# Optimization experiments

Measured on AMD Instinct MI355X. Metric: run time of the kernel, lower is better.

## Reference

```python
import jax, jax.numpy as jnp
import numpy as np

NUM_HEADS = 12


def setup_inputs() -> dict:
    key = jax.random.key(0)
    ks = jax.random.split(key, 6)
    B, T, D = 512, 128, 768  # batch, seq (<= CONTEXT_LENGTH=128), d_model
    d_in, d_out = D, D
    s_in = 1.0 / np.sqrt(d_in)
    s_out = 1.0 / np.sqrt(d_out)
    return {
        "x": jax.random.normal(ks[0], (B, T, d_in), dtype=jnp.float32),
        "Wq": jax.random.uniform(ks[1], (d_in, d_out), jnp.float32, -s_in, s_in),
        "Wk": jax.random.uniform(ks[2], (d_in, d_out), jnp.float32, -s_in, s_in),
        "Wv": jax.random.uniform(ks[3], (d_in, d_out), jnp.float32, -s_in, s_in),
        "Wo": jax.random.uniform(ks[4], (d_out, d_out), jnp.float32, -s_out, s_out),
        "bo": jax.random.uniform(ks[5], (d_out,), jnp.float32, -s_out, s_out),
    }


def reference(x, Wq, Wk, Wv, Wo, bo):
    B, T, _ = x.shape
    H = NUM_HEADS
    hd = Wq.shape[1] // H
    # projections -> [b, h, t, hd]
    q = jnp.einsum("btd,de->bte", x, Wq).reshape(B, T, H, hd).transpose(0, 2, 1, 3)
    k = jnp.einsum("btd,de->bte", x, Wk).reshape(B, T, H, hd).transpose(0, 2, 1, 3)
    v = jnp.einsum("btd,de->bte", x, Wv).reshape(B, T, H, hd).transpose(0, 2, 1, 3)
    scores = jnp.einsum("bhqd,bhkd->bhqk", q, k)
    causal = jnp.tril(jnp.ones((T, T), dtype=bool))  # True = keep
    scores = jnp.where(causal, scores, -jnp.inf)
    attn = jax.nn.softmax(scores / jnp.sqrt(jnp.float32(hd)), axis=-1)
    # dropout is identity in eval mode
    ctx = jnp.einsum("bhqk,bhkd->bhqd", attn, v)
    ctx = ctx.transpose(0, 2, 1, 3).reshape(B, T, H * hd)
    return jnp.einsum("btd,de->bte", ctx, Wo) + bo
```

## Files before the change

### kernel.cpp

```cpp
#include <hip/hip_runtime.h>
#include <hip/hip_bf16.h>
#include <cstdint>
#include <math.h>


typedef __bf16 bf16;
typedef __bf16 bf16x8 __attribute__((ext_vector_type(8)));
typedef float f32x4 __attribute__((ext_vector_type(4)));

#define MFMA16(a, b, c) __builtin_amdgcn_mfma_f32_16x16x32_bf16((a), (b), (c), 0, 0, 0)

#define GLD_LDS16(gp, lp)                                                       \
  __builtin_amdgcn_global_load_lds(                                             \
      (const __attribute__((address_space(1))) void*)(gp),                      \
      (__attribute__((address_space(3))) void*)(lp), 16, 0, 0)

__global__ __launch_bounds__(256) void cast_x_bf16(const float* __restrict__ in,
                                                   bf16* __restrict__ out, int n) {
  int i = (blockIdx.x * 256 + threadIdx.x) * 4;
  if (i < n) {
    float4 v = *(const float4*)(in + i);
    bf16 o[4] = {(bf16)v.x, (bf16)v.y, (bf16)v.z, (bf16)v.w};
    *(uint2*)(out + i) = *(const uint2*)o;
  }
}

__global__ __launch_bounds__(256) void transpose_cast_w(const float* __restrict__ W,
                                                        bf16* __restrict__ Out) {
  __shared__ float t[32][33];
  int bx = blockIdx.x * 32;
  int by = blockIdx.y * 32;
  int tx = threadIdx.x, ty = threadIdx.y;
  for (int i = 0; i < 32; i += 8)
    t[ty + i][tx] = W[(size_t)(bx + ty + i) * 768 + by + tx];
  __syncthreads();
  for (int i = 0; i < 32; i += 8)
    Out[(size_t)(by + ty + i) * 768 + bx + tx] = (bf16)t[tx][ty + i];
}

template <bool OUT_F32>
__global__ __launch_bounds__(512, 2) void gemm256(
    const bf16* __restrict__ A, int lda, const bf16* __restrict__ Bt, int ldb,
    void* __restrict__ Cout, int ldc, const float* __restrict__ bias, int K,
    int ntn) {
  __shared__ bf16 smem[4 * 16384];

  const int tid = threadIdx.x;
  const int lane = tid & 63;
  const int w = tid >> 6;

  const int nwg = gridDim.x;
  const int wg = (blockIdx.x & 7) * (nwg >> 3) + (blockIdx.x >> 3);
  const int m0 = (wg / ntn) * 256;
  const int n0 = (wg % ntn) * 256;

  const int r0 = tid >> 2;
  const int c0 = ((((tid & 3) * 16) ^ (((tid >> 3) & 3) << 4)) >> 1);
  const bf16* Ablk = A + (size_t)m0 * lda;
  const bf16* Bblk = Bt + (size_t)n0 * ldb;

  const int lm = lane & 15;
  const int kqs = ((lane >> 4) * 8) ^ (((lm >> 1) & 3) << 3);
  const int wm = (w & 1) * 128;
  const int wn = (w >> 1) * 64;

  f32x4 acc[8][4];
#pragma unroll
  for (int i = 0; i < 8; ++i)
#pragma unroll
    for (int j = 0; j < 4; ++j) acc[i][j] = (f32x4){0.f, 0.f, 0.f, 0.f};

  const int NT = K >> 5;

#define STAGE(t)                                                                  \
  {                                                                               \
    bf16* sb = smem + ((t) & 3) * 16384;                                          \
    const int k0 = (t) * 32;                                                      \
    GLD_LDS16(Ablk + (size_t)r0 * lda + k0 + c0, sb + w * 512);                   \
    GLD_LDS16(Ablk + (size_t)(128 + r0) * lda + k0 + c0, sb + 4096 + w * 512);    \
    GLD_LDS16(Bblk + (size_t)r0 * ldb + k0 + c0, sb + 8192 + w * 512);            \
    GLD_LDS16(Bblk + (size_t)(128 + r0) * ldb + k0 + c0, sb + 12288 + w * 512);   \
  }

  STAGE(0);
  STAGE(1);
  STAGE(2);
  asm volatile("s_waitcnt vmcnt(8)" ::: "memory");
  __builtin_amdgcn_s_barrier();
  __builtin_amdgcn_sched_barrier(0);

  for (int t = 0; t < NT; ++t) {
    if (t + 3 < NT) STAGE(t + 3);

    const bf16* base = smem + (t & 3) * 16384;
    bf16x8 af[8], bfr[4];
#pragma unroll
    for (int mi = 0; mi < 8; ++mi)
      af[mi] = *(const bf16x8*)(base + (wm + mi * 16 + lm) * 32 + kqs);
#pragma unroll
    for (int ni = 0; ni < 4; ++ni)
      bfr[ni] = *(const bf16x8*)(base + 8192 + (wn + ni * 16 + lm) * 32 + kqs);

    __builtin_amdgcn_s_setprio(1);
#pragma unroll
    for (int mi = 0; mi < 8; ++mi)
#pragma unroll
      for (int ni = 0; ni < 4; ++ni)
        acc[mi][ni] = MFMA16(af[mi], bfr[ni], acc[mi][ni]);
    __builtin_amdgcn_s_setprio(0);

    if (t + 3 < NT)
      asm volatile("s_waitcnt vmcnt(8)" ::: "memory");
    else if (t + 3 == NT)
      asm volatile("s_waitcnt vmcnt(4)" ::: "memory");
    else
      asm volatile("s_waitcnt vmcnt(0)" ::: "memory");
    __builtin_amdgcn_s_barrier();
    __builtin_amdgcn_sched_barrier(0);
  }
#undef STAGE

  const int lr = (lane >> 4) * 4;
#pragma unroll
  for (int mi = 0; mi < 8; ++mi)
#pragma unroll
    for (int ni = 0; ni < 4; ++ni) {
      const int col = n0 + wn + ni * 16 + lm;
#pragma unroll
      for (int r = 0; r < 4; ++r) {
        const int row = m0 + wm + mi * 16 + lr + r;
        if constexpr (OUT_F32)
          ((float*)Cout)[(size_t)row * ldc + col] = acc[mi][ni][r] + bias[col];
        else
          ((bf16*)Cout)[(size_t)row * ldc + col] = (bf16)acc[mi][ni][r];
      }
    }
}

__global__ __launch_bounds__(256) void attn_kernel(const bf16* __restrict__ qkv,
                                                   bf16* __restrict__ ctx) {
  constexpr int LDQ = 2304;
  constexpr int SQS = 72;
  constexpr int SPS = 136;
  __shared__ bf16 smem[27136];
  bf16* sQ = smem;
  bf16* sK = smem + 128 * SQS;
  bf16* sVt = smem + 2 * 128 * SQS;
  bf16* sP = smem;

  const int bh = blockIdx.x;
  const int b = bh / 12, h = bh % 12;
  const bf16* Qg = qkv + (size_t)b * 128 * LDQ + h * 64;
  const bf16* Kg = Qg + 768;
  const bf16* Vg = Qg + 1536;

  const int tid = threadIdx.x;
  {
    int row = tid >> 1, half = tid & 1;
    const uint4* qsrc = (const uint4*)(Qg + (size_t)row * LDQ + half * 32);
    const uint4* ksrc = (const uint4*)(Kg + (size_t)row * LDQ + half * 32);
    const uint4* vsrc = (const uint4*)(Vg + (size_t)row * LDQ + half * 32);
    uint4* qdst = (uint4*)(sQ + row * SQS + half * 32);
    uint4* kdst = (uint4*)(sK + row * SQS + half * 32);
    uint4 vt[4];
    for (int i = 0; i < 4; ++i) {
      qdst[i] = qsrc[i];
      kdst[i] = ksrc[i];
      vt[i] = vsrc[i];
    }
    const bf16* tp = (const bf16*)vt;
    for (int d = 0; d < 32; ++d) sVt[(half * 32 + d) * SPS + row] = tp[d];
  }
  __syncthreads();

  const int lane = tid & 63;
  const int w = tid >> 6;
  const int lm = lane & 15;
  const int kq = (lane >> 4) * 8;
  const int lr = (lane >> 4) * 4;

  f32x4 sacc[2][8];
  for (int i = 0; i < 2; ++i)
    for (int j = 0; j < 8; ++j) sacc[i][j] = (f32x4){0.f, 0.f, 0.f, 0.f};
  for (int kk = 0; kk < 64; kk += 32) {
    bf16x8 aq[2], bk[8];
    for (int mi = 0; mi < 2; ++mi)
      aq[mi] = *(const bf16x8*)(sQ + (w * 32 + mi * 16 + lm) * SQS + kk + kq);
    for (int ni = 0; ni < 8; ++ni)
      bk[ni] = *(const bf16x8*)(sK + (ni * 16 + lm) * SQS + kk + kq);
    for (int mi = 0; mi < 2; ++mi)
      for (int ni = 0; ni < 8; ++ni)
        sacc[mi][ni] = MFMA16(aq[mi], bk[ni], sacc[mi][ni]);
  }

  float inv[2][4];
  for (int mi = 0; mi < 2; ++mi) {
    for (int r = 0; r < 4; ++r) {
      int row = w * 32 + mi * 16 + lr + r;
      float vals[8];
      float mx = -INFINITY;
      for (int ni = 0; ni < 8; ++ni) {
        int col = ni * 16 + lm;
        float v = sacc[mi][ni][r] * 0.125f;
        if (col > row) v = -INFINITY;
        vals[ni] = v;
        mx = fmaxf(mx, v);
      }
      for (int off = 1; off < 16; off <<= 1) mx = fmaxf(mx, __shfl_xor(mx, off, 64));
      float sum = 0.f;
      for (int ni = 0; ni < 8; ++ni) {
        float p = __expf(vals[ni] - mx);
        vals[ni] = p;
        sum += p;
      }
      for (int off = 1; off < 16; off <<= 1) sum += __shfl_xor(sum, off, 64);
      inv[mi][r] = 1.f / sum;
      for (int ni = 0; ni < 8; ++ni) sacc[mi][ni][r] = vals[ni];
    }
  }
  __syncthreads();

  for (int mi = 0; mi < 2; ++mi)
    for (int ni = 0; ni < 8; ++ni)
      for (int r = 0; r < 4; ++r) {
        int row = w * 32 + mi * 16 + lr + r;
        int col = ni * 16 + lm;
        sP[row * SPS + col] = (bf16)sacc[mi][ni][r];
      }
  __syncthreads();

  f32x4 oacc[2][4];
  for (int i = 0; i < 2; ++i)
    for (int j = 0; j < 4; ++j) oacc[i][j] = (f32x4){0.f, 0.f, 0.f, 0.f};
  for (int kk = 0; kk < 128; kk += 32) {
    bf16x8 ap[2], bv[4];
    for (int mi = 0; mi < 2; ++mi)
      ap[mi] = *(const bf16x8*)(sP + (w * 32 + mi * 16 + lm) * SPS + kk + kq);
    for (int ci = 0; ci < 4; ++ci)
      bv[ci] = *(const bf16x8*)(sVt + (ci * 16 + lm) * SPS + kk + kq);
    for (int mi = 0; mi < 2; ++mi)
      for (int ci = 0; ci < 4; ++ci)
        oacc[mi][ci] = MFMA16(ap[mi], bv[ci], oacc[mi][ci]);
  }

  bf16* Cg = ctx + (size_t)b * 128 * LDQ + h * 64;
  for (int mi = 0; mi < 2; ++mi)
    for (int ci = 0; ci < 4; ++ci)
      for (int r = 0; r < 4; ++r) {
        int row = w * 32 + mi * 16 + lr + r;
        int col = ci * 16 + lm;
        Cg[(size_t)row * LDQ + col] = (bf16)(oacc[mi][ci][r] * inv[mi][r]);
      }
}

extern "C" void kernel_launch(void* const* d_in, const int* in_sizes, int n_in,
                              void* d_out, int out_size, void* d_ws, size_t ws_size,
                              hipStream_t stream) {
  const float* x = (const float*)d_in[0];
  const float* Wq = (const float*)d_in[1];
  const float* Wk = (const float*)d_in[2];
  const float* Wv = (const float*)d_in[3];
  const float* Wo = (const float*)d_in[4];
  const float* bo = (const float*)d_in[5];
  float* out = (float*)d_out;

  constexpr int M = 512 * 128;
  constexpr int D = 768;
  constexpr size_t XB_BYTES = (size_t)M * D * 2;
  constexpr size_t WQKV_BYTES = (size_t)3 * D * D * 2;
  constexpr size_t WOT_BYTES = (size_t)D * D * 2;

  char* ws = (char*)d_ws;
  bf16* xb = (bf16*)ws;
  bf16* wqkv = (bf16*)(ws + XB_BYTES);
  bf16* wot = (bf16*)(ws + XB_BYTES + WQKV_BYTES);
  bf16* qkv = (bf16*)(ws + XB_BYTES + WQKV_BYTES + WOT_BYTES);

  cast_x_bf16<<<(M * D) / 1024, 256, 0, stream>>>(x, xb, M * D);
  dim3 tb(32, 8);
  transpose_cast_w<<<dim3(24, 24), tb, 0, stream>>>(Wq, wqkv);
  transpose_cast_w<<<dim3(24, 24), tb, 0, stream>>>(Wk, wqkv + 768 * 768);
  transpose_cast_w<<<dim3(24, 24), tb, 0, stream>>>(Wv, wqkv + 2 * 768 * 768);
  transpose_cast_w<<<dim3(24, 24), tb, 0, stream>>>(Wo, wot);
  gemm256<false><<<dim3(2304), 512, 0, stream>>>(xb, 768, wqkv, 768, qkv, 2304,
                                                 nullptr, 768, 9);
  attn_kernel<<<512 * 12, 256, 0, stream>>>(qkv, qkv);
  gemm256<true><<<dim3(768), 512, 0, stream>>>(qkv, 2304, wot, 768, out, 768,
                                               bo, 768, 3);
}
```

Before: 795.3 us.

## Restructure GEMM into finer-grained double-buffered pipeline with LDS-staged coalesced epilogue

Reworks the GEMM main loop from a 4-stage, 32-wide K ring into two 64-wide K buffers split into half-steps. Each half-step interleaves global-to-LDS prefetch, fragment reads for half the M tile and 16 MFMAs, which shrinks register pressure and spreads the loads more evenly. The epilogue now stages results through swizzled LDS so global stores become 16-byte coalesced writes instead of scattered scalar stores. The attention grid index is remapped so that consecutive blocks are spread across XCDs. The cost is many more barriers per K step and added complexity in the waitcnt accounting.

```diff
diff --git a/kernel.cpp b/kernel.cpp
--- a/kernel.cpp
+++ b/kernel.cpp
@@ -43,7 +43,7 @@
     const bf16* __restrict__ A, int lda, const bf16* __restrict__ Bt, int ldb,
     void* __restrict__ Cout, int ldc, const float* __restrict__ bias, int K,
     int ntn) {
-  __shared__ bf16 smem[4 * 16384];
+  __shared__ bf16 smem[2 * 32768];
 
   const int tid = threadIdx.x;
   const int lane = tid & 63;
@@ -56,13 +56,17 @@
 
   const int r0 = tid >> 2;
   const int c0 = ((((tid & 3) * 16) ^ (((tid >> 3) & 3) << 4)) >> 1);
-  const bf16* Ablk = A + (size_t)m0 * lda;
-  const bf16* Bblk = Bt + (size_t)n0 * ldb;
+  const bf16* As0 = A + (size_t)(m0 + r0) * lda + c0;
+  const bf16* As1 = As0 + (size_t)128 * lda;
+  const bf16* Bs0 = Bt + (size_t)(n0 + r0) * ldb + c0;
+  const bf16* Bs1 = Bs0 + (size_t)128 * ldb;
 
   const int lm = lane & 15;
   const int kqs = ((lane >> 4) * 8) ^ (((lm >> 1) & 3) << 3);
   const int wm = (w & 1) * 128;
   const int wn = (w >> 1) * 64;
+  const bf16* pA = smem + (wm + lm) * 32 + kqs;
+  const bf16* pB = smem + 16384 + (wn + lm) * 32 + kqs;
 
   f32x4 acc[8][4];
 #pragma unroll
@@ -70,71 +74,137 @@
 #pragma unroll
     for (int j = 0; j < 4; ++j) acc[i][j] = (f32x4){0.f, 0.f, 0.f, 0.f};
 
-  const int NT = K >> 5;
-
-#define STAGE(t)                                                                  \
-  {                                                                               \
-    bf16* sb = smem + ((t) & 3) * 16384;                                          \
-    const int k0 = (t) * 32;                                                      \
-    GLD_LDS16(Ablk + (size_t)r0 * lda + k0 + c0, sb + w * 512);                   \
-    GLD_LDS16(Ablk + (size_t)(128 + r0) * lda + k0 + c0, sb + 4096 + w * 512);    \
-    GLD_LDS16(Bblk + (size_t)r0 * ldb + k0 + c0, sb + 8192 + w * 512);            \
-    GLD_LDS16(Bblk + (size_t)(128 + r0) * ldb + k0 + c0, sb + 12288 + w * 512);   \
-  }
-
-  STAGE(0);
-  STAGE(1);
-  STAGE(2);
-  asm volatile("s_waitcnt vmcnt(8)" ::: "memory");
+  bf16x8 af[4], bfr[4];
+
+  const int NT = K >> 6;
+  const int NH = NT >> 1;
+
+  auto SA = [&](int t, int kh) {
+    const int ko = t * 64 + kh * 32;
+    const int lo = (t & 1) * 32768 + kh * 8192;
+    GLD_LDS16(As0 + ko, smem + lo + w * 512);
+    GLD_LDS16(As1 + ko, smem + lo + 4096 + w * 512);
+  };
+  auto SB = [&](int t, int kh) {
+    const int ko = t * 64 + kh * 32;
+    const int lo = (t & 1) * 32768 + 16384 + kh * 8192;
+    GLD_LDS16(Bs0 + ko, smem + lo + w * 512);
+    GLD_LDS16(Bs1 + ko, smem + lo + 4096 + w * 512);
+  };
+  auto RD = [&](int buf, int kh, int h, bool lb) {
+    const bf16* a = pA + buf * 32768 + kh * 8192 + h * 2048;
+#pragma unroll
+    for (int j = 0; j < 4; ++j) af[j] = *(const bf16x8*)(a + j * 512);
+    if (lb) {
+      const bf16* b = pB + buf * 32768 + kh * 8192;
+#pragma unroll
+      for (int j = 0; j < 4; ++j) bfr[j] = *(const bf16x8*)(b + j * 512);
+    }
+  };
+  auto BARMID = [&](int vm) {
+    if (vm == 6) asm volatile("s_waitcnt vmcnt(6)" ::: "memory");
+    else if (vm == 0) asm volatile("s_waitcnt vmcnt(0)" ::: "memory");
+    __builtin_amdgcn_s_barrier();
+    asm volatile("s_waitcnt lgkmcnt(0)" ::: "memory");
+    __builtin_amdgcn_sched_barrier(0);
+  };
+  auto BAREND = [&]() {
+    __builtin_amdgcn_s_barrier();
+    __builtin_amdgcn_sched_barrier(0);
+  };
+  auto MM = [&](int h) {
+    __builtin_amdgcn_s_setprio(1);
+#pragma unroll
+    for (int j = 0; j < 4; ++j)
+#pragma unroll
+      for (int n = 0; n < 4; ++n)
+        acc[h * 4 + j][n] = MFMA16(af[j], bfr[n], acc[h * 4 + j][n]);
+    __builtin_amdgcn_s_setprio(0);
+  };
+
+  SB(0, 0); SA(0, 0); SB(0, 1); SA(0, 1);
+  asm volatile("s_waitcnt vmcnt(4)" ::: "memory");
+  SB(1, 0); SA(1, 0); SB(1, 1);
+  asm volatile("s_waitcnt vmcnt(6)" ::: "memory");
   __builtin_amdgcn_s_barrier();
   __builtin_amdgcn_sched_barrier(0);
 
-  for (int t = 0; t < NT; ++t) {
-    if (t + 3 < NT) STAGE(t + 3);
-
-    const bf16* base = smem + (t & 3) * 16384;
-    bf16x8 af[8], bfr[4];
+  for (int i = 0; i < NH - 1; ++i) {
+    const int t1 = 2 * i + 1, t2 = 2 * i + 2, t3 = 2 * i + 3;
+    RD(0, 0, 0, true);  SA(t1, 1); BARMID(-1); MM(0); BAREND();
+    RD(0, 0, 1, false); SB(t2, 0); BARMID(-1); MM(1); BAREND();
+    RD(0, 1, 0, true);  SA(t2, 0); BARMID(-1); MM(0); BAREND();
+    RD(0, 1, 1, false); SB(t2, 1); BARMID(6);  MM(1); BAREND();
+    RD(1, 0, 0, true);  SA(t2, 1); BARMID(-1); MM(0); BAREND();
+    RD(1, 0, 1, false); SB(t3, 0); BARMID(-1); MM(1); BAREND();
+    RD(1, 1, 0, true);  SA(t3, 0); BARMID(-1); MM(0); BAREND();
+    RD(1, 1, 1, false); SB(t3, 1); BARMID(6);  MM(1); BAREND();
+  }
+  RD(0, 0, 0, true);  SA(NT - 1, 1); BARMID(-1); MM(0); BAREND();
+  RD(0, 0, 1, false);                BARMID(-1); MM(1); BAREND();
+  RD(0, 1, 0, true);                 BARMID(-1); MM(0); BAREND();
+  RD(0, 1, 1, false);                BARMID(0);  MM(1); BAREND();
+  RD(1, 0, 0, true);                 BARMID(-1); MM(0); BAREND();
+  RD(1, 0, 1, false);                BARMID(-1); MM(1); BAREND();
+  RD(1, 1, 0, true);                 BARMID(-1); MM(0); BAREND();
+  RD(1, 1, 1, false);                BARMID(-1); MM(1); BAREND();
+
+  __syncthreads();
+
+  const int lr = (lane >> 4) * 4;
+  if constexpr (!OUT_F32) {
+    const unsigned exw = (unsigned)(lane >> 4) << 5;
 #pragma unroll
     for (int mi = 0; mi < 8; ++mi)
-      af[mi] = *(const bf16x8*)(base + (wm + mi * 16 + lm) * 32 + kqs);
-#pragma unroll
-    for (int ni = 0; ni < 4; ++ni)
-      bfr[ni] = *(const bf16x8*)(base + 8192 + (wn + ni * 16 + lm) * 32 + kqs);
-
-    __builtin_amdgcn_s_setprio(1);
-#pragma unroll
-    for (int mi = 0; mi < 8; ++mi)
-#pragma unroll
-      for (int ni = 0; ni < 4; ++ni)
-        acc[mi][ni] = MFMA16(af[mi], bfr[ni], acc[mi][ni]);
-    __builtin_amdgcn_s_setprio(0);
-
-    if (t + 3 < NT)
-      asm volatile("s_waitcnt vmcnt(8)" ::: "memory");
-    else if (t + 3 == NT)
-      asm volatile("s_waitcnt vmcnt(4)" ::: "memory");
-    else
-      asm volatile("s_waitcnt vmcnt(0)" ::: "memory");
-    __builtin_amdgcn_s_barrier();
-    __builtin_amdgcn_sched_barrier(0);
-  }
-#undef STAGE
-
-  const int lr = (lane >> 4) * 4;
-#pragma unroll
-  for (int mi = 0; mi < 8; ++mi)
-#pragma unroll
-    for (int ni = 0; ni < 4; ++ni) {
-      const int col = n0 + wn + ni * 16 + lm;
-#pragma unroll
-      for (int r = 0; r < 4; ++r) {
-        const int row = m0 + wm + mi * 16 + lr + r;
-        if constexpr (OUT_F32)
-          ((float*)Cout)[(size_t)row * ldc + col] = acc[mi][ni][r] + bias[col];
-        else
-          ((bf16*)Cout)[(size_t)row * ldc + col] = (bf16)acc[mi][ni][r];
-      }
-    }
+#pragma unroll
+      for (int ni = 0; ni < 4; ++ni) {
+        const int colb = (wn + ni * 16 + lm) * 2;
+#pragma unroll
+        for (int r = 0; r < 4; ++r) {
+          const unsigned ad = (unsigned)(wm + mi * 16 + lr + r) * 512 + colb;
+          *(bf16*)((char*)smem + (ad ^ exw)) = (bf16)acc[mi][ni][r];
+        }
+      }
+    __syncthreads();
+    const unsigned exr = (unsigned)((tid >> 7) & 3) << 5;
+#pragma unroll
+    for (int s = 0; s < 16; ++s) {
+      const int e = s * 4096 + tid * 8;
+      const int row = e >> 8, col = e & 255;
+      uint4 v = *(const uint4*)((char*)smem + (((unsigned)row * 512 + col * 2) ^ exr));
+      *(uint4*)((bf16*)Cout + (size_t)(m0 + row) * ldc + n0 + col) = v;
+    }
+  } else {
+    const unsigned exw = (unsigned)(lane >> 4) << 6;
+#pragma unroll
+    for (int h = 0; h < 2; ++h) {
+      __syncthreads();
+      if ((w & 1) == h) {
+#pragma unroll
+        for (int mi = 0; mi < 8; ++mi)
+#pragma unroll
+          for (int ni = 0; ni < 4; ++ni) {
+            const int colb = (wn + ni * 16 + lm) * 4;
+#pragma unroll
+            for (int r = 0; r < 4; ++r) {
+              const unsigned ad = (unsigned)(mi * 16 + lr + r) * 1024 + colb;
+              *(float*)((char*)smem + (ad ^ exw)) = acc[mi][ni][r];
+            }
+          }
+      }
+      __syncthreads();
+#pragma unroll
+      for (int s = 0; s < 16; ++s) {
+        const int row = s * 8 + w;
+        const int col = (lane & 63) * 4;
+        const unsigned xr = (unsigned)((row >> 2) & 3) << 6;
+        float4 v = *(const float4*)((char*)smem + (((unsigned)row * 1024 + col * 4) ^ xr));
+        float4 bb = *(const float4*)(bias + n0 + col);
+        v.x += bb.x; v.y += bb.y; v.z += bb.z; v.w += bb.w;
+        *(float4*)((float*)Cout + (size_t)(m0 + h * 128 + row) * ldc + n0 + col) = v;
+      }
+    }
+  }
 }
 
 __global__ __launch_bounds__(256) void attn_kernel(const bf16* __restrict__ qkv,
@@ -148,7 +218,7 @@
   bf16* sVt = smem + 2 * 128 * SQS;
   bf16* sP = smem;
 
-  const int bh = blockIdx.x;
+  const int bh = (blockIdx.x & 7) * 768 + (blockIdx.x >> 3);
   const int b = bh / 12, h = bh % 12;
   const bf16* Qg = qkv + (size_t)b * 128 * LDQ + h * 64;
   const bf16* Kg = Qg + 768;
```

Result: no change. 788.8 us (-0.8%).
